# Performance work log

Hardware: AMD Instinct MI355X
Metric: run time of the kernel (lower is better)

Reference implementation:

```python
import jax, jax.numpy as jnp
import numpy as np

B, D, E, H = 2048, 1024, 16, 4096
NUM_ACTIVE = 2
LN_EPS = 1e-5
NORM_EPS = 1e-12


def setup_inputs() -> dict:
    key = jax.random.key(0)
    ks = jax.random.split(key, 4)
    s1 = 1.0 / np.sqrt(D)
    s2 = 1.0 / np.sqrt(H)
    return {
        "input": jax.random.normal(ks[0], (B, D), jnp.float32),
        "ln_gamma": jnp.ones((D,), jnp.float32),
        "ln_beta": jnp.zeros((D,), jnp.float32),
        "expert_keys": jax.random.normal(ks[1], (D, E), jnp.float32),
        "W1": jax.random.normal(ks[2], (E, D, H), jnp.float32) * s1,
        "b1": jnp.zeros((E, H), jnp.float32),
        "W2": jax.random.normal(ks[3], (E, H, D), jnp.float32) * s2,
        "b2": jnp.zeros((E, D), jnp.float32),
    }


def reference(input, ln_gamma, ln_beta, expert_keys, W1, b1, W2, b2):
    # Gating: LayerNorm(input) @ normalize(expert_keys, dim=-1)
    mu = jnp.mean(input, axis=-1, keepdims=True)
    var = jnp.mean((input - mu) ** 2, axis=-1, keepdims=True)
    xn = (input - mu) / jnp.sqrt(var + LN_EPS) * ln_gamma + ln_beta
    # F.normalize(expert_keys, dim=-1): each row (per feature) normalized over experts
    keys = expert_keys / jnp.clip(
        jnp.linalg.norm(expert_keys, axis=-1, keepdims=True), NORM_EPS)
    logits = xn @ keys  # [B, E]
    # Top-k routing (argsort descending, take first num_active)
    top_vals, top_ids = jax.lax.top_k(logits, NUM_ACTIVE)  # [B, k]
    gates_k = jax.nn.softmax(top_vals, axis=-1)            # softmax over chosen logits
    gates = jnp.zeros_like(logits).at[
        jnp.arange(logits.shape[0])[:, None], top_ids].set(gates_k)  # [B, E]
    # Experts applied to RAW input (not the normalized gating input), dense-all-experts
    h = jax.nn.relu(jnp.einsum('bd,edh->beh', input, W1) + b1)   # [B, E, H]
    eo = jnp.einsum('beh,ehd->bed', h, W2) + b2                  # [B, E, D]
    # Weighted combine: only top-k experts have nonzero gates
    out = jnp.einsum('bed,be->bd', eo, gates)                    # [B, D]
    return out
```

## Files before the change

### kernel.cpp

```cpp
#include <hip/hip_runtime.h>
#include <hip/hip_bf16.h>
#include <cstdint>
#include <cstddef>

#define D_ 1024
#define H_ 4096
#define E_ 16
#define B_ 2048

constexpr int CAP = 384;

typedef __attribute__((ext_vector_type(4))) float f32x4;
typedef __attribute__((ext_vector_type(8))) short bf16x8;

__device__ __forceinline__ unsigned pack2(float a, float b) {
  __hip_bfloat162 h = __float22bfloat162_rn(make_float2(a, b));
  union { __hip_bfloat162 h2; unsigned u; } cv; cv.h2 = h;
  return cv.u;
}
__device__ __forceinline__ float bflo(unsigned u) { return __uint_as_float(u << 16); }
__device__ __forceinline__ float bfhi(unsigned u) { return __uint_as_float(u & 0xffff0000u); }

#define GLL16(g, l)                                                         \
  __builtin_amdgcn_global_load_lds(                                         \
      (const __attribute__((address_space(1))) void*)(g),                   \
      (__attribute__((address_space(3))) void*)(l), 16, 0, 0)

#define WAITV(n) asm volatile("s_waitcnt vmcnt(" #n ")" ::: "memory")
#define BAR() __builtin_amdgcn_s_barrier()

__global__ void moe_zero(int* __restrict__ cnt) {
  if (threadIdx.x < E_) cnt[threadIdx.x] = 0;
}

__global__ __launch_bounds__(256) void moe_gating3(
    const float* __restrict__ x, const float* __restrict__ gamma,
    const float* __restrict__ beta, const float* __restrict__ keys,
    int* __restrict__ cnt, int4* __restrict__ rmi, float2* __restrict__ rmg,
    unsigned short* __restrict__ xg)
{
  const int b = blockIdx.x, t = threadIdx.x;
  const int w = t >> 6;
  const float4 xv = ((const float4*)(x + (size_t)b * D_))[t];
  float s  = xv.x + xv.y + xv.z + xv.w;
  float sq = xv.x*xv.x + xv.y*xv.y + xv.z*xv.z + xv.w*xv.w;
#pragma unroll
  for (int off = 32; off >= 1; off >>= 1) {
    s  += __shfl_down(s, off);
    sq += __shfl_down(sq, off);
  }
  __shared__ float ssum[4], ssq[4], sstat[2];
  if ((t & 63) == 0) { ssum[w] = s; ssq[w] = sq; }
  __syncthreads();
  if (t == 0) {
    float S = ssum[0] + ssum[1] + ssum[2] + ssum[3];
    float Q = ssq[0] + ssq[1] + ssq[2] + ssq[3];
    float mu  = S * (1.0f / D_);
    float var = Q * (1.0f / D_) - mu * mu;
    sstat[0] = mu; sstat[1] = rsqrtf(var + 1e-5f);
  }
  __syncthreads();
  const float mu = sstat[0], rstd = sstat[1];
  const float4 gv = ((const float4*)gamma)[t];
  const float4 bv = ((const float4*)beta)[t];
  float xn[4] = {(xv.x-mu)*rstd*gv.x+bv.x, (xv.y-mu)*rstd*gv.y+bv.y,
                 (xv.z-mu)*rstd*gv.z+bv.z, (xv.w-mu)*rstd*gv.w+bv.w};
  float acc[E_];
#pragma unroll
  for (int e2 = 0; e2 < E_; ++e2) acc[e2] = 0.f;
#pragma unroll
  for (int j = 0; j < 4; ++j) {
    const int d = 4*t + j;
    const float* kr = keys + (size_t)d * E_;
    float kv[E_];
#pragma unroll
    for (int e2 = 0; e2 < E_; ++e2) kv[e2] = kr[e2];
    float nq = 0.f;
#pragma unroll
    for (int e2 = 0; e2 < E_; ++e2) nq += kv[e2] * kv[e2];
    const float sc = xn[j] / fmaxf(sqrtf(nq), 1e-12f);
#pragma unroll
    for (int e2 = 0; e2 < E_; ++e2) acc[e2] += sc * kv[e2];
  }
#pragma unroll
  for (int off = 1; off < 64; off <<= 1) {
#pragma unroll
    for (int e2 = 0; e2 < E_; ++e2) acc[e2] += __shfl_xor(acc[e2], off);
  }
  __shared__ float wred[4][E_];
  if ((t & 63) == 0) {
#pragma unroll
    for (int e2 = 0; e2 < E_; ++e2) wred[w][e2] = acc[e2];
  }
  __syncthreads();
  __shared__ int sE[2], sP[2];
  if (t == 0) {
    float lg[E_];
#pragma unroll
    for (int e2 = 0; e2 < E_; ++e2)
      lg[e2] = wred[0][e2] + wred[1][e2] + wred[2][e2] + wred[3][e2];
    float v0 = -1e30f; int e0 = 0;
    for (int e2 = 0; e2 < E_; ++e2) { if (lg[e2] > v0) { v0 = lg[e2]; e0 = e2; } }
    float v1 = -1e30f; int e1 = 0;
    for (int e2 = 0; e2 < E_; ++e2) { if (e2 == e0) continue; if (lg[e2] > v1) { v1 = lg[e2]; e1 = e2; } }
    const float g0 = 1.f / (1.f + __expf(v1 - v0));
    const float g1 = 1.f - g0;
    int p0 = atomicAdd(cnt + e0, 1); if (p0 >= CAP) p0 = CAP - 1;
    int p1 = atomicAdd(cnt + e1, 1); if (p1 >= CAP) p1 = CAP - 1;
    rmi[b] = make_int4(e0, p0, e1, p1);
    rmg[b] = make_float2(g0, g1);
    sE[0] = e0; sP[0] = p0;
    sE[1] = e1; sP[1] = p1;
  }
  __syncthreads();
  const uint2 pk = make_uint2(pack2(xv.x, xv.y), pack2(xv.z, xv.w));
#pragma unroll
  for (int i = 0; i < 2; ++i)
    ((uint2*)(xg + ((size_t)sE[i] * CAP + sP[i]) * D_))[t] = pk;
}

template<int KROW, int KLEN, int WN, int SPLITK, bool RELU>
__global__ void __launch_bounds__(256, 4)
moe_gemm(const unsigned short* __restrict__ Asrc, const float* __restrict__ W,
         const float* __restrict__ bias, const int* __restrict__ cnt,
         unsigned short* __restrict__ d0, unsigned short* __restrict__ d1,
         unsigned short* __restrict__ d2, unsigned short* __restrict__ d3)
{
  constexpr int NPHASE = KLEN / 32;
  constexpr int NT = WN / 64;
  constexpr int MT = 2;

  const int bx = blockIdx.x;
  const int xcd = bx & 7;
  int slot = bx >> 3;
  const int mt = slot % MT; slot /= MT;
  const int nt = slot % NT; slot /= NT;
  const int eh = slot & 1;  slot >>= 1;
  const int part = slot;
  const int e  = (xcd << 1) | eh;
  const int nb = nt * 64;
  const int koff = part * KLEN;
  unsigned short* dst = (part == 0) ? d0 : (part == 1) ? d1 : (part == 2) ? d2 : d3;

  int cntE = cnt[e]; if (cntE > CAP) cntE = CAP;
  if (mt * 192 >= cntE) return;

  const int t = threadIdx.x, w = t >> 6, lane = t & 63;
  const int l15 = lane & 15, l4 = lane >> 4;

  __shared__ __align__(16) unsigned short As[2][192 * 32];
  __shared__ __align__(16) float Bs[2][2048];

  asm volatile("s_waitcnt vmcnt(0) lgkmcnt(0)" ::: "memory");

  const unsigned short* Ae = Asrc + (size_t)e * CAP * KROW + (size_t)mt * 192 * KROW + koff;
  const float* We = W + (size_t)e * KROW * WN + (size_t)koff * WN + nb;

  const unsigned short *srcA0, *srcA1, *srcA2;
  {
    const int c0 = t,        r0 = c0 >> 2;
    const int c1 = t + 256,  r1 = c1 >> 2;
    const int c2 = t + 512,  r2 = c2 >> 2;
    srcA0 = Ae + (size_t)r0 * KROW + ((c0 & 3) ^ ((r0 >> 1) & 3)) * 8;
    srcA1 = Ae + (size_t)r1 * KROW + ((c1 & 3) ^ ((r1 >> 1) & 3)) * 8;
    srcA2 = Ae + (size_t)r2 * KROW + ((c2 & 3) ^ ((r2 >> 1) & 3)) * 8;
  }
  const float *srcB0, *srcB1;
  {
    const int kr0 = w * 8 + (lane >> 4);
    const int c4  = (lane & 15) ^ (w << 2);
    srcB0 = We + (size_t)kr0 * WN + c4 * 4;
    srcB1 = srcB0 + (size_t)4 * WN;
  }

#define ISSUE(p, BUF) do {                                                  \
    const int ko_ = (p) * 32;                                               \
    GLL16(srcA0 + ko_, &As[BUF][(0 * 256 + w * 64) * 8]);                   \
    GLL16(srcA1 + ko_, &As[BUF][(1 * 256 + w * 64) * 8]);                   \
    GLL16(srcA2 + ko_, &As[BUF][(2 * 256 + w * 64) * 8]);                   \
    GLL16(srcB0 + (size_t)ko_ * WN, &Bs[BUF][w * 512]);                     \
    GLL16(srcB1 + (size_t)ko_ * WN, &Bs[BUF][w * 512 + 256]);               \
  } while (0)

  f32x4 acc[12];
#pragma unroll
  for (int rf = 0; rf < 12; ++rf) acc[rf] = f32x4{0,0,0,0};

  const int swA = (l15 >> 1) & 3;
  const int mrow0 = mt * 192;
  const int ncol = w * 16 + l15;
  const int bslot = (ncol >> 2) ^ (l4 << 2);
  const int bbase = bslot * 4 + (ncol & 3);

#define COMP(BUF) do {                                                      \
    float bfv[8];                                                           \
    _Pragma("unroll")                                                       \
    for (int j2 = 0; j2 < 8; ++j2)                                          \
      bfv[j2] = Bs[BUF][(l4 * 8 + j2) * 64 + bbase];                        \
    union { unsigned u[4]; bf16x8 v; } BB;                                  \
    _Pragma("unroll")                                                       \
    for (int i2 = 0; i2 < 4; ++i2)                                          \
      BB.u[i2] = pack2(bfv[2*i2], bfv[2*i2+1]);                             \
    __builtin_amdgcn_s_setprio(1);                                          \
    _Pragma("unroll")                                                       \
    for (int rf = 0; rf < 12; ++rf) {                                       \
      if (mrow0 + rf * 16 < cntE) {                                         \
        const bf16x8 a = *(const bf16x8*)&As[BUF][((rf * 16 + l15) * 4 + (l4 ^ swA)) * 8]; \
        acc[rf] = __builtin_amdgcn_mfma_f32_16x16x32_bf16(a, BB.v, acc[rf], 0,0,0); \
      }                                                                     \
    }                                                                       \
    __builtin_amdgcn_s_setprio(0);                                          \
  } while (0)

  ISSUE(0, 0);
#pragma unroll 1
  for (int p = 0; p < NPHASE; p += 2) {
    ISSUE(p + 1, 1);
    WAITV(5);
    BAR(); COMP(0); BAR();
    if (p + 2 < NPHASE) { ISSUE(p + 2, 0); WAITV(5); }
    else { WAITV(0); }
    BAR(); COMP(1); BAR();
  }
#undef ISSUE
#undef COMP

  unsigned short* dbase = dst + (size_t)e * CAP * WN + nb + w * 16;
  float bv = 0.f;
  if constexpr (RELU) bv = bias[e * WN + nb + w * 16 + l15];
#pragma unroll
  for (int rf = 0; rf < 12; ++rf) {
    if (mrow0 + rf * 16 >= cntE && rf > 0) continue;
#pragma unroll
    for (int r = 0; r < 4; ++r) {
      const int row = mrow0 + rf * 16 + l4 * 4 + r;
      float v = acc[rf][r];
      if constexpr (RELU) v = fmaxf(v + bv, 0.f);
      const unsigned u01 = pack2(v, __shfl_xor(v, 1));
      const float uo = __shfl_xor(__uint_as_float(u01), 2);
      if ((l15 & 3) == 0)
        *(uint2*)(dbase + (size_t)row * WN + l15) = make_uint2(u01, __float_as_uint(uo));
    }
  }
}

__global__ __launch_bounds__(256) void moe_comb(
    const unsigned short* __restrict__ p0, const unsigned short* __restrict__ p1,
    const unsigned short* __restrict__ p2, const unsigned short* __restrict__ p3,
    const float* __restrict__ b2, const int4* __restrict__ rmi,
    const float2* __restrict__ rmg, float* __restrict__ out)
{
  const int b = blockIdx.x, t = threadIdx.x;
  const int4 m = rmi[b];
  const float2 g = rmg[b];
  const int c = t * 4;
  const size_t offA = ((size_t)m.x * CAP + m.y) * D_ + c;
  const size_t offB = ((size_t)m.z * CAP + m.w) * D_ + c;
  float a0, a1, a2, a3, c0, c1, c2, c3;
  {
    const uint2 ua = *(const uint2*)(p0 + offA);
    const uint2 ub = *(const uint2*)(p0 + offB);
    a0 = bflo(ua.x); a1 = bfhi(ua.x); a2 = bflo(ua.y); a3 = bfhi(ua.y);
    c0 = bflo(ub.x); c1 = bfhi(ub.x); c2 = bflo(ub.y); c3 = bfhi(ub.y);
  }
  const unsigned short* parts[3] = { p1, p2, p3 };
#pragma unroll
  for (int i = 0; i < 3; ++i) {
    if (parts[i] != nullptr) {
      const uint2 ua = *(const uint2*)(parts[i] + offA);
      const uint2 ub = *(const uint2*)(parts[i] + offB);
      a0 += bflo(ua.x); a1 += bfhi(ua.x); a2 += bflo(ua.y); a3 += bfhi(ua.y);
      c0 += bflo(ub.x); c1 += bfhi(ub.x); c2 += bflo(ub.y); c3 += bfhi(ub.y);
    }
  }
  const float4 b2a = *(const float4*)(b2 + (size_t)m.x * D_ + c);
  const float4 b2b = *(const float4*)(b2 + (size_t)m.z * D_ + c);
  float4 o;
  o.x = g.x * (a0 + b2a.x) + g.y * (c0 + b2b.x);
  o.y = g.x * (a1 + b2a.y) + g.y * (c1 + b2b.y);
  o.z = g.x * (a2 + b2a.z) + g.y * (c2 + b2b.z);
  o.w = g.x * (a3 + b2a.w) + g.y * (c3 + b2b.w);
  *(float4*)(out + (size_t)b * D_ + c) = o;
}

extern "C" void kernel_launch(void* const* d_in, const int* in_sizes, int n_in,
                              void* d_out, int out_size, void* d_ws, size_t ws_size,
                              hipStream_t stream) {
  const float* x     = (const float*)d_in[0];
  const float* gamma = (const float*)d_in[1];
  const float* beta  = (const float*)d_in[2];
  const float* keys  = (const float*)d_in[3];
  const float* W1    = (const float*)d_in[4];
  const float* b1    = (const float*)d_in[5];
  const float* W2    = (const float*)d_in[6];
  const float* b2    = (const float*)d_in[7];
  float* out = (float*)d_out;

  char* ws = (char*)d_ws;
  const size_t OFF_RMI = 256;
  const size_t OFF_RMG = OFF_RMI + (size_t)B_ * 16;
  const size_t OFF_XG  = OFF_RMG + (size_t)B_ * 8;
  const size_t EO_SZ   = (size_t)E_ * CAP * D_ * 2;
  const size_t OFF_HW  = OFF_XG + EO_SZ;
  const size_t HW_SZ   = (size_t)E_ * CAP * H_ * 2;
  const size_t OFF_EO1 = OFF_HW + HW_SZ;
  const size_t NEED2   = OFF_EO1 + EO_SZ;
  const size_t NEED4   = OFF_EO1 + 3 * EO_SZ;

  int*    cnt = (int*)ws;
  int4*   rmi = (int4*)(ws + OFF_RMI);
  float2* rmg = (float2*)(ws + OFF_RMG);
  unsigned short* xg  = (unsigned short*)(ws + OFF_XG);
  unsigned short* eo0 = xg;
  unsigned short* hws = (unsigned short*)(ws + OFF_HW);

  moe_zero<<<1, 64, 0, stream>>>(cnt);
  moe_gating3<<<B_, 256, 0, stream>>>(x, gamma, beta, keys, cnt, rmi, rmg, xg);

  moe_gemm<D_, D_, H_, 1, true><<<2048, 256, 0, stream>>>(
      xg, W1, b1, cnt, hws, nullptr, nullptr, nullptr);

  if (ws_size >= NEED4) {
    unsigned short* eo1 = (unsigned short*)(ws + OFF_EO1);
    unsigned short* eo2 = (unsigned short*)(ws + OFF_EO1 + EO_SZ);
    unsigned short* eo3 = (unsigned short*)(ws + OFF_EO1 + 2 * EO_SZ);
    moe_gemm<H_, H_ / 4, D_, 4, false><<<2048, 256, 0, stream>>>(
        hws, W2, nullptr, cnt, eo0, eo1, eo2, eo3);
    moe_comb<<<B_, 256, 0, stream>>>(eo0, eo1, eo2, eo3, b2, rmi, rmg, out);
  } else if (ws_size >= NEED2) {
    unsigned short* eo1 = (unsigned short*)(ws + OFF_EO1);
    moe_gemm<H_, H_ / 2, D_, 2, false><<<1024, 256, 0, stream>>>(
        hws, W2, nullptr, cnt, eo0, eo1, nullptr, nullptr);
    moe_comb<<<B_, 256, 0, stream>>>(eo0, eo1, nullptr, nullptr, b2, rmi, rmg, out);
  } else {
    moe_gemm<H_, H_, D_, 1, false><<<512, 256, 0, stream>>>(
        hws, W2, nullptr, cnt, eo0, nullptr, nullptr, nullptr);
    moe_comb<<<B_, 256, 0, stream>>>(eo0, nullptr, nullptr, nullptr, b2, rmi, rmg, out);
  }
}
```

Measured before the change: 333.5 us.

## Retile expert GEMM to 128x128 with register-staged bf16 B tiles in LDS

Changes the expert GEMM tile from 192x64 to 128x128 (three M tiles, two N fragments per wave). W is now loaded into registers as fp32, converted to bf16 once, and written to LDS in an MFMA-ready swizzled layout. Before, fp32 W went into LDS through global_load_lds and every wave repacked it on each read. This gives more B reuse per A load and removes the repeated conversion, at the cost of more registers (launch bounds lowered to 3), strided per-thread global loads of W, and a more complex pipelining schedule.

```diff
diff --git a/kernel.cpp b/kernel.cpp
--- a/kernel.cpp
+++ b/kernel.cpp
@@ -27,6 +27,8 @@
       (__attribute__((address_space(3))) void*)(l), 16, 0, 0)
 
 #define WAITV(n) asm volatile("s_waitcnt vmcnt(" #n ")" ::: "memory")
+#define WAITL()  asm volatile("s_waitcnt lgkmcnt(0)" ::: "memory")
+#define MEMBAR() asm volatile("" ::: "memory")
 #define BAR() __builtin_amdgcn_s_barrier()
 
 __global__ void moe_zero(int* __restrict__ cnt) {
@@ -120,15 +122,15 @@
 }
 
 template<int KROW, int KLEN, int WN, int SPLITK, bool RELU>
-__global__ void __launch_bounds__(256, 4)
+__global__ void __launch_bounds__(256, 3)
 moe_gemm(const unsigned short* __restrict__ Asrc, const float* __restrict__ W,
          const float* __restrict__ bias, const int* __restrict__ cnt,
          unsigned short* __restrict__ d0, unsigned short* __restrict__ d1,
          unsigned short* __restrict__ d2, unsigned short* __restrict__ d3)
 {
   constexpr int NPHASE = KLEN / 32;
-  constexpr int NT = WN / 64;
-  constexpr int MT = 2;
+  constexpr int NT = WN / 128;
+  constexpr int MT = 3;
 
   const int bx = blockIdx.x;
   const int xcd = bx & 7;
@@ -138,108 +140,136 @@
   const int eh = slot & 1;  slot >>= 1;
   const int part = slot;
   const int e  = (xcd << 1) | eh;
-  const int nb = nt * 64;
+  const int nb = nt * 128;
   const int koff = part * KLEN;
   unsigned short* dst = (part == 0) ? d0 : (part == 1) ? d1 : (part == 2) ? d2 : d3;
 
   int cntE = cnt[e]; if (cntE > CAP) cntE = CAP;
-  if (mt * 192 >= cntE) return;
+  if (mt * 128 >= cntE) return;
 
   const int t = threadIdx.x, w = t >> 6, lane = t & 63;
   const int l15 = lane & 15, l4 = lane >> 4;
 
-  __shared__ __align__(16) unsigned short As[2][192 * 32];
-  __shared__ __align__(16) float Bs[2][2048];
+  __shared__ __align__(16) unsigned short As[2][128 * 32];
+  __shared__ __align__(16) unsigned short Bs[2][128 * 32];
 
   asm volatile("s_waitcnt vmcnt(0) lgkmcnt(0)" ::: "memory");
 
-  const unsigned short* Ae = Asrc + (size_t)e * CAP * KROW + (size_t)mt * 192 * KROW + koff;
+  const unsigned short* Ae = Asrc + (size_t)e * CAP * KROW + (size_t)mt * 128 * KROW + koff;
   const float* We = W + (size_t)e * KROW * WN + (size_t)koff * WN + nb;
 
-  const unsigned short *srcA0, *srcA1, *srcA2;
+  const unsigned short *srcA0, *srcA1;
   {
     const int c0 = t,        r0 = c0 >> 2;
     const int c1 = t + 256,  r1 = c1 >> 2;
-    const int c2 = t + 512,  r2 = c2 >> 2;
     srcA0 = Ae + (size_t)r0 * KROW + ((c0 & 3) ^ ((r0 >> 1) & 3)) * 8;
     srcA1 = Ae + (size_t)r1 * KROW + ((c1 & 3) ^ ((r1 >> 1) & 3)) * 8;
-    srcA2 = Ae + (size_t)r2 * KROW + ((c2 & 3) ^ ((r2 >> 1) & 3)) * 8;
-  }
-  const float *srcB0, *srcB1;
-  {
-    const int kr0 = w * 8 + (lane >> 4);
-    const int c4  = (lane & 15) ^ (w << 2);
-    srcB0 = We + (size_t)kr0 * WN + c4 * 4;
-    srcB1 = srcB0 + (size_t)4 * WN;
-  }
-
-#define ISSUE(p, BUF) do {                                                  \
+  }
+  const int bn = t & 127, bkh = t >> 7;
+  const float* srcB = We + (size_t)(bkh * 16) * WN + bn;
+  const int bo0 = bn * 64 + (((bkh * 2 + 0) ^ ((bn >> 1) & 3)) << 4);
+  const int bo1 = bn * 64 + (((bkh * 2 + 1) ^ ((bn >> 1) & 3)) << 4);
+
+  float R0[16], R1[16];
+
+#define ISSUE_A(p, BUF) do {                                                \
     const int ko_ = (p) * 32;                                               \
     GLL16(srcA0 + ko_, &As[BUF][(0 * 256 + w * 64) * 8]);                   \
     GLL16(srcA1 + ko_, &As[BUF][(1 * 256 + w * 64) * 8]);                   \
-    GLL16(srcA2 + ko_, &As[BUF][(2 * 256 + w * 64) * 8]);                   \
-    GLL16(srcB0 + (size_t)ko_ * WN, &Bs[BUF][w * 512]);                     \
-    GLL16(srcB1 + (size_t)ko_ * WN, &Bs[BUF][w * 512 + 256]);               \
   } while (0)
 
-  f32x4 acc[12];
-#pragma unroll
-  for (int rf = 0; rf < 12; ++rf) acc[rf] = f32x4{0,0,0,0};
+#define ISSUE_B(p, Rv) do {                                                 \
+    const float* bp_ = srcB + (size_t)(p) * 32 * WN;                        \
+    _Pragma("unroll")                                                       \
+    for (int j = 0; j < 16; ++j)                                            \
+      Rv[j] = bp_[(size_t)j * WN];                                          \
+  } while (0)
+
+#define WRITE(Rv, BUF) do {                                                 \
+    uint4 q0_, q1_;                                                         \
+    q0_.x = pack2(Rv[0],  Rv[1]);  q0_.y = pack2(Rv[2],  Rv[3]);            \
+    q0_.z = pack2(Rv[4],  Rv[5]);  q0_.w = pack2(Rv[6],  Rv[7]);            \
+    q1_.x = pack2(Rv[8],  Rv[9]);  q1_.y = pack2(Rv[10], Rv[11]);           \
+    q1_.z = pack2(Rv[12], Rv[13]); q1_.w = pack2(Rv[14], Rv[15]);           \
+    *(uint4*)((char*)&Bs[BUF][0] + bo0) = q0_;                              \
+    *(uint4*)((char*)&Bs[BUF][0] + bo1) = q1_;                              \
+  } while (0)
+
+  f32x4 acc[8][2];
+#pragma unroll
+  for (int rf = 0; rf < 8; ++rf) { acc[rf][0] = f32x4{0,0,0,0}; acc[rf][1] = f32x4{0,0,0,0}; }
 
   const int swA = (l15 >> 1) & 3;
-  const int mrow0 = mt * 192;
-  const int ncol = w * 16 + l15;
-  const int bslot = (ncol >> 2) ^ (l4 << 2);
-  const int bbase = bslot * 4 + (ncol & 3);
+  const int mrow0 = mt * 128;
 
 #define COMP(BUF) do {                                                      \
-    float bfv[8];                                                           \
+    bf16x8 BB[2];                                                           \
     _Pragma("unroll")                                                       \
-    for (int j2 = 0; j2 < 8; ++j2)                                          \
-      bfv[j2] = Bs[BUF][(l4 * 8 + j2) * 64 + bbase];                        \
-    union { unsigned u[4]; bf16x8 v; } BB;                                  \
-    _Pragma("unroll")                                                       \
-    for (int i2 = 0; i2 < 4; ++i2)                                          \
-      BB.u[i2] = pack2(bfv[2*i2], bfv[2*i2+1]);                             \
+    for (int cf = 0; cf < 2; ++cf) {                                        \
+      const int n_ = w * 32 + cf * 16 + l15;                                \
+      BB[cf] = *(const bf16x8*)((const char*)&Bs[BUF][0]                    \
+               + (n_ * 64 + ((l4 ^ ((n_ >> 1) & 3)) << 4)));                \
+    }                                                                       \
     __builtin_amdgcn_s_setprio(1);                                          \
     _Pragma("unroll")                                                       \
-    for (int rf = 0; rf < 12; ++rf) {                                       \
+    for (int rf = 0; rf < 8; ++rf) {                                        \
       if (mrow0 + rf * 16 < cntE) {                                         \
         const bf16x8 a = *(const bf16x8*)&As[BUF][((rf * 16 + l15) * 4 + (l4 ^ swA)) * 8]; \
-        acc[rf] = __builtin_amdgcn_mfma_f32_16x16x32_bf16(a, BB.v, acc[rf], 0,0,0); \
+        acc[rf][0] = __builtin_amdgcn_mfma_f32_16x16x32_bf16(a, BB[0], acc[rf][0], 0,0,0); \
+        acc[rf][1] = __builtin_amdgcn_mfma_f32_16x16x32_bf16(a, BB[1], acc[rf][1], 0,0,0); \
       }                                                                     \
     }                                                                       \
     __builtin_amdgcn_s_setprio(0);                                          \
   } while (0)
 
-  ISSUE(0, 0);
+  ISSUE_A(0, 0); MEMBAR();
+  ISSUE_B(0, R0); MEMBAR();
+  ISSUE_B(1, R1);
 #pragma unroll 1
   for (int p = 0; p < NPHASE; p += 2) {
-    ISSUE(p + 1, 1);
-    WAITV(5);
-    BAR(); COMP(0); BAR();
-    if (p + 2 < NPHASE) { ISSUE(p + 2, 0); WAITV(5); }
-    else { WAITV(0); }
-    BAR(); COMP(1); BAR();
-  }
-#undef ISSUE
+    if (p + 1 < NPHASE) { WAITV(16); } else { WAITV(0); }
+    WRITE(R0, 0);
+    if (p + 1 < NPHASE) { ISSUE_A(p + 1, 1); }
+    MEMBAR();
+    if (p + 2 < NPHASE) { ISSUE_B(p + 2, R0); }
+    WAITL(); BAR();
+    COMP(0);
+    BAR();
+    if (p + 1 < NPHASE) {
+      if (p + 2 < NPHASE) { WAITV(16); } else { WAITV(0); }
+      WRITE(R1, 1);
+      if (p + 2 < NPHASE) { ISSUE_A(p + 2, 0); }
+      MEMBAR();
+      if (p + 3 < NPHASE) { ISSUE_B(p + 3, R1); }
+      WAITL(); BAR();
+      COMP(1);
+      BAR();
+    }
+  }
+#undef ISSUE_A
+#undef ISSUE_B
+#undef WRITE
 #undef COMP
 
-  unsigned short* dbase = dst + (size_t)e * CAP * WN + nb + w * 16;
-  float bv = 0.f;
-  if constexpr (RELU) bv = bias[e * WN + nb + w * 16 + l15];
-#pragma unroll
-  for (int rf = 0; rf < 12; ++rf) {
+  unsigned short* dbase = dst + (size_t)e * CAP * WN + nb + w * 32;
+#pragma unroll
+  for (int rf = 0; rf < 8; ++rf) {
     if (mrow0 + rf * 16 >= cntE && rf > 0) continue;
 #pragma unroll
-    for (int r = 0; r < 4; ++r) {
-      const int row = mrow0 + rf * 16 + l4 * 4 + r;
-      float v = acc[rf][r];
-      if constexpr (RELU) v = fmaxf(v + bv, 0.f);
-      const unsigned u01 = pack2(v, __shfl_xor(v, 1));
-      const float uo = __shfl_xor(__uint_as_float(u01), 2);
-      if ((l15 & 3) == 0)
-        *(uint2*)(dbase + (size_t)row * WN + l15) = make_uint2(u01, __float_as_uint(uo));
+    for (int cf = 0; cf < 2; ++cf) {
+      float bv = 0.f;
+      if constexpr (RELU) bv = bias[e * WN + nb + w * 32 + cf * 16 + l15];
+#pragma unroll
+      for (int r = 0; r < 4; ++r) {
+        const int row = mrow0 + rf * 16 + l4 * 4 + r;
+        float v = acc[rf][cf][r];
+        if constexpr (RELU) v = fmaxf(v + bv, 0.f);
+        const unsigned u01 = pack2(v, __shfl_xor(v, 1));
+        const float uo = __shfl_xor(__uint_as_float(u01), 2);
+        if ((l15 & 3) == 0)
+          *(uint2*)(dbase + (size_t)row * WN + cf * 16 + l15) =
+              make_uint2(u01, __float_as_uint(uo));
+      }
     }
   }
 }
@@ -317,23 +347,23 @@
   moe_zero<<<1, 64, 0, stream>>>(cnt);
   moe_gating3<<<B_, 256, 0, stream>>>(x, gamma, beta, keys, cnt, rmi, rmg, xg);
 
-  moe_gemm<D_, D_, H_, 1, true><<<2048, 256, 0, stream>>>(
+  moe_gemm<D_, D_, H_, 1, true><<<1536, 256, 0, stream>>>(
       xg, W1, b1, cnt, hws, nullptr, nullptr, nullptr);
 
   if (ws_size >= NEED4) {
     unsigned short* eo1 = (unsigned short*)(ws + OFF_EO1);
     unsigned short* eo2 = (unsigned short*)(ws + OFF_EO1 + EO_SZ);
     unsigned short* eo3 = (unsigned short*)(ws + OFF_EO1 + 2 * EO_SZ);
-    moe_gemm<H_, H_ / 4, D_, 4, false><<<2048, 256, 0, stream>>>(
+    moe_gemm<H_, H_ / 4, D_, 4, false><<<1536, 256, 0, stream>>>(
         hws, W2, nullptr, cnt, eo0, eo1, eo2, eo3);
     moe_comb<<<B_, 256, 0, stream>>>(eo0, eo1, eo2, eo3, b2, rmi, rmg, out);
   } else if (ws_size >= NEED2) {
     unsigned short* eo1 = (unsigned short*)(ws + OFF_EO1);
-    moe_gemm<H_, H_ / 2, D_, 2, false><<<1024, 256, 0, stream>>>(
+    moe_gemm<H_, H_ / 2, D_, 2, false><<<768, 256, 0, stream>>>(
         hws, W2, nullptr, cnt, eo0, eo1, nullptr, nullptr);
     moe_comb<<<B_, 256, 0, stream>>>(eo0, eo1, nullptr, nullptr, b2, rmi, rmg, out);
   } else {
-    moe_gemm<H_, H_, D_, 1, false><<<512, 256, 0, stream>>>(
+    moe_gemm<H_, H_, D_, 1, false><<<384, 256, 0, stream>>>(
         hws, W2, nullptr, cnt, eo0, nullptr, nullptr, nullptr);
     moe_comb<<<B_, 256, 0, stream>>>(eo0, nullptr, nullptr, nullptr, b2, rmi, rmg, out);
   }
```

Result: faster. 297.0 us (-10.9%).
